# Optimization experiments

Measured on AMD Instinct MI355X. Metric: run time of the kernel, lower is better.

## Reference

```python
import jax, jax.numpy as jnp
import numpy as np

B, S, D = 64, 1024, 128
EPS = 1e-5

def hardswish(x):
    return x * jnp.clip(x + 3.0, 0.0, 6.0) / 6.0

def setup_inputs() -> dict:
    key = jax.random.key(0)
    k1, k2, k3 = jax.random.split(key, 3)
    x = jax.random.normal(k1, (B, S, D), dtype=jnp.float32)
    ln_w = jnp.ones((S, D), dtype=jnp.float32)
    ln_b = jnp.zeros((S, D), dtype=jnp.float32)
    # U1[i]/U2[i] rows packed into lower-triangular (S,S); init ~ N(0,1)*0.01
    W1 = jax.random.normal(k2, (S, S), dtype=jnp.float32) * 0.01
    W2 = jax.random.normal(k3, (S, S), dtype=jnp.float32) * 0.01
    return {"x": x, "ln_w": ln_w, "ln_b": ln_b, "W1": W1, "W2": W2}

def reference(x, ln_w, ln_b, W1, W2):
    # LayerNorm over the last two dims (seq_len, feature_dim) jointly
    mu = jnp.mean(x, axis=(-2, -1), keepdims=True)
    var = jnp.mean(jnp.square(x - mu), axis=(-2, -1), keepdims=True)
    h = (x - mu) * jax.lax.rsqrt(var + EPS) * ln_w + ln_b
    # causal (lower-triangular) time mixing: u[:, t] = sum_{s<=t} W1[t, s] * h[:, s]
    mask = jnp.tril(jnp.ones((S, S), dtype=x.dtype))
    u = hardswish(jnp.einsum('ts,bsd->btd', W1 * mask, h))
    v = jnp.einsum('ts,bsd->btd', W2 * mask, u)
    return x + v
```

## Files before the change

### kernel.cpp

```cpp
#include <hip/hip_runtime.h>
#include <hip/hip_bf16.h>

#define NB 64
#define S_ 1024
#define D_ 128

typedef __attribute__((ext_vector_type(8))) short bf16x8;
typedef __attribute__((ext_vector_type(4))) float f32x4;


__device__ __forceinline__ unsigned short f2bf(float f) {
  __hip_bfloat16 h = __float2bfloat16(f);
  return __builtin_bit_cast(unsigned short, h);
}

__device__ __forceinline__ void async_copy16(const void* g, void* l) {
  __builtin_amdgcn_global_load_lds(
      (const __attribute__((address_space(1))) unsigned int*)g,
      (__attribute__((address_space(3))) unsigned int*)l, 16, 0, 0);
}

__global__ __launch_bounds__(256) void init_stats(unsigned* __restrict__ c) {
#pragma unroll
  for (int i = 0; i < 8; ++i) c[threadIdx.x + i * 256] = 0u;
}

__global__ __launch_bounds__(256) void prep_norm_kernel(
    const float* __restrict__ x, const float* __restrict__ ln_w,
    const float* __restrict__ ln_b, const float* __restrict__ W1,
    const float* __restrict__ W2, float* __restrict__ stats,
    unsigned short* __restrict__ W1f, unsigned short* __restrict__ W2f,
    unsigned short* __restrict__ hTf) {
  __shared__ __align__(16) unsigned short lds[64 * 132 + 32];
  float2* w4 = (float2*)(lds + 64 * 132);
  float* mr = (float*)(lds + 64 * 132 + 16);

  const int blk = blockIdx.x;
  const int b = blk >> 4;
  const int s0 = (blk & 15) * 64;
  const int t = threadIdx.x;
  const int wave = t >> 6, lane = t & 63;
  const int quad = lane >> 4, l16 = lane & 15;

  float* sb = stats + (size_t)b * 32;
  unsigned* cntp = (unsigned*)sb + 2;

  const float4* xb = (const float4*)(x + ((size_t)b * S_ + s0) * D_);
  {
    float s = 0.f, q = 0.f;
#pragma unroll
    for (int i = 0; i < 8; ++i) {
      float4 v = xb[i * 256 + t];
      s += v.x + v.y + v.z + v.w;
      q += v.x * v.x + v.y * v.y + v.z * v.z + v.w * v.w;
    }
#pragma unroll
    for (int o = 32; o > 0; o >>= 1) {
      s += __shfl_down(s, o, 64);
      q += __shfl_down(q, o, 64);
    }
    if (lane == 0) w4[wave] = make_float2(s, q);
  }
  __syncthreads();
  if (t == 0) {
    float ss = 0.f, qq = 0.f;
#pragma unroll
    for (int i = 0; i < 4; ++i) { ss += w4[i].x; qq += w4[i].y; }
    float o1 = __hip_atomic_fetch_add(sb + 0, ss, __ATOMIC_RELAXED,
                                      __HIP_MEMORY_SCOPE_AGENT);
    float o2 = __hip_atomic_fetch_add(sb + 1, qq, __ATOMIC_RELAXED,
                                      __HIP_MEMORY_SCOPE_AGENT);
    asm volatile("" ::"v"(o1), "v"(o2));
    __hip_atomic_fetch_add(cntp, 1u, __ATOMIC_RELAXED,
                           __HIP_MEMORY_SCOPE_AGENT);
  }

  {
    const int u = blk * 4 + wave;
    const int f = u & 2047;
    const int p = f >> 5, c = f & 31;
    const int r = p * 16 + l16;
    const int k0 = c * 32 + quad * 8;
    const float* wsrc = ((u >> 11) ? W2 : W1) + (size_t)r * 1024 + k0;
    float4 a0 = ((const float4*)wsrc)[0];
    float4 a1 = ((const float4*)wsrc)[1];
    float av[8] = {a0.x, a0.y, a0.z, a0.w, a1.x, a1.y, a1.z, a1.w};
    bf16x8 o;
#pragma unroll
    for (int jj = 0; jj < 8; ++jj)
      o[jj] = (short)f2bf((k0 + jj <= r) ? av[jj] : 0.f);
    unsigned short* dstp = ((u >> 11) ? W2f : W1f) +
                           ((size_t)p * 32 + c) * 512 + lane * 8;
    *(bf16x8*)dstp = o;
  }

  if (t == 0) {
    int guard = 0;
    while (__hip_atomic_load(cntp, __ATOMIC_RELAXED,
                             __HIP_MEMORY_SCOPE_AGENT) < 16u) {
      __builtin_amdgcn_s_sleep(4);
      if (++guard > 400000) break;
    }
    float s1 = __hip_atomic_load(sb + 0, __ATOMIC_RELAXED,
                                 __HIP_MEMORY_SCOPE_AGENT);
    float s2 = __hip_atomic_load(sb + 1, __ATOMIC_RELAXED,
                                 __HIP_MEMORY_SCOPE_AGENT);
    const float inv = 1.0f / (S_ * D_);
    const float mu = s1 * inv;
    mr[0] = mu;
    mr[1] = rsqrtf(s2 * inv - mu * mu + 1e-5f);
  }
  __syncthreads();
  const float mu = mr[0];
  const float rs = mr[1];

  const float4* wb = (const float4*)(ln_w + (size_t)s0 * D_);
  const float4* bv4 = (const float4*)(ln_b + (size_t)s0 * D_);
#pragma unroll
  for (int r = 0; r < 8; ++r) {
    const int f = r * 256 + t;
    const int srow = f >> 5;
    const int c4 = f & 31;
    float4 xv = xb[f];
    float4 wv = wb[f];
    float4 bvv = bv4[f];
    ushort4 o;
    o.x = f2bf((xv.x - mu) * rs * wv.x + bvv.x);
    o.y = f2bf((xv.y - mu) * rs * wv.y + bvv.y);
    o.z = f2bf((xv.z - mu) * rs * wv.z + bvv.z);
    o.w = f2bf((xv.w - mu) * rs * wv.w + bvv.w);
    *(ushort4*)(lds + srow * 132 + c4 * 4) = o;
  }
  __syncthreads();
  unsigned short* outp = hTf + (size_t)b * (D_ * S_);
  const int cg0 = (blk & 15) * 2;
#pragma unroll
  for (int ff = 0; ff < 4; ++ff) {
    const int f = wave * 4 + ff;
    const int p = f >> 1, cl = f & 1;
    const int d = p * 16 + l16;
    const int sbase = cl * 32 + quad * 8;
    bf16x8 v;
#pragma unroll
    for (int jj = 0; jj < 8; ++jj)
      v[jj] = (short)lds[(sbase + jj) * 132 + d];
    *(bf16x8*)(outp + ((size_t)p * 32 + cg0 + cl) * 512 + lane * 8) = v;
  }
}

template <bool HSWISH>
__global__ __launch_bounds__(256, 4) void gemm_causal(
    const unsigned short* __restrict__ Af, const unsigned short* __restrict__ Bf,
    unsigned short* __restrict__ Uf, const float* __restrict__ Xres,
    float* __restrict__ Out) {
  __shared__ __align__(16) unsigned short ldsA[16384];

  const int t = threadIdx.x;
  const int wave = t >> 6, lane = t & 63;
  const int quad = lane >> 4, l16 = lane & 15;

  const int bi = blockIdx.x;
  const int xcd = bi & 7;
  const int slot = bi >> 3;
  const int b = xcd * 8 + (slot & 7);
  const int j = slot >> 3;
  const int mt = (j < 8) ? j : (j ^ 3);
  const int row0 = mt * 64;

  const int cend = 2 * (mt + 1);
  const int npan = (cend + 7) >> 3;

  const unsigned short* Ab = Af + (size_t)mt * 4 * 32 * 512;
  const unsigned short* Bb = Bf + (size_t)b * (D_ * S_);

  f32x4 acc[4][2] = {};
  bf16x8 Bp[4][2];
#pragma unroll
  for (int g = 0; g < 4; ++g) {
    const int gg = (g < cend) ? g : 0;
#pragma unroll
    for (int jj = 0; jj < 2; ++jj)
      Bp[g][jj] = *(const bf16x8*)(Bb + ((size_t)(wave * 2 + jj) * 32 + gg) * 512 + lane * 8);
  }

  for (int p = 0; p < npan; ++p) {
    if (p) __syncthreads();
    const int rem = cend - p * 8;
#pragma unroll
    for (int jc = 0; jc < 8; ++jc) {
      const int flat16 = jc * 256 + t;
      const int iw = flat16 >> 9;
      const int cc = (flat16 >> 6) & 7;
      const int li = flat16 & 63;
      if (cc < rem)
        async_copy16(Ab + ((size_t)iw * 32 + p * 8 + cc) * 512 + li * 8,
                     ldsA + flat16 * 8);
    }
    __syncthreads();
#pragma unroll
    for (int c = 0; c < 8; ++c) {
      const int g = p * 8 + c;
      if (g < cend) {
        bf16x8 af[4];
#pragma unroll
        for (int i = 0; i < 4; ++i)
          af[i] = *(const bf16x8*)(ldsA + i * 4096 + c * 512 + lane * 8);
        __builtin_amdgcn_s_setprio(1);
#pragma unroll
        for (int i = 0; i < 4; ++i)
#pragma unroll
          for (int jj = 0; jj < 2; ++jj)
            acc[i][jj] = __builtin_amdgcn_mfma_f32_16x16x32_bf16(
                af[i], Bp[c & 3][jj], acc[i][jj], 0, 0, 0);
        __builtin_amdgcn_s_setprio(0);
        const int gn = (g + 4 < cend) ? (g + 4) : 0;
#pragma unroll
        for (int jj = 0; jj < 2; ++jj)
          Bp[c & 3][jj] = *(const bf16x8*)(
              Bb + ((size_t)(wave * 2 + jj) * 32 + gn) * 512 + lane * 8);
      }
    }
  }

  if (HSWISH) {
    __syncthreads();
    unsigned short* ldsT = ldsA;
#pragma unroll
    for (int i = 0; i < 4; ++i)
#pragma unroll
      for (int jj = 0; jj < 2; ++jj) {
        ushort4 pk;
        float v0 = acc[i][jj][0], v1 = acc[i][jj][1], v2 = acc[i][jj][2], v3 = acc[i][jj][3];
        pk.x = f2bf(v0 * fminf(fmaxf(v0 + 3.f, 0.f), 6.f) * (1.f / 6.f));
        pk.y = f2bf(v1 * fminf(fmaxf(v1 + 3.f, 0.f), 6.f) * (1.f / 6.f));
        pk.z = f2bf(v2 * fminf(fmaxf(v2 + 3.f, 0.f), 6.f) * (1.f / 6.f));
        pk.w = f2bf(v3 * fminf(fmaxf(v3 + 3.f, 0.f), 6.f) * (1.f / 6.f));
        const int n = wave * 32 + jj * 16 + l16;
        const int m0 = i * 16 + quad * 4;
        *(ushort4*)(ldsT + n * 72 + m0) = pk;
      }
    __syncthreads();
    unsigned short* gU = Uf + (size_t)b * (D_ * S_);
#pragma unroll
    for (int ff = 0; ff < 4; ++ff) {
      const int f = wave * 4 + ff;
      const int p2 = f >> 1, cl = f & 1;
      const int d = p2 * 16 + l16;
      const int tb = cl * 32 + quad * 8;
      bf16x8 v = *(const bf16x8*)(ldsT + d * 72 + tb);
      *(bf16x8*)(gU + ((size_t)p2 * 32 + mt * 2 + cl) * 512 + lane * 8) = v;
    }
  } else {
    float* gO = Out + (size_t)b * S_ * D_;
    const float* gX = Xres + (size_t)b * S_ * D_;
#pragma unroll
    for (int i = 0; i < 4; ++i) {
      const int mrow0 = row0 + i * 16 + quad * 4;
#pragma unroll
      for (int jj = 0; jj < 2; ++jj) {
        const int col = wave * 32 + jj * 16 + l16;
#pragma unroll
        for (int r = 0; r < 4; ++r) {
          const int addr = (mrow0 + r) * D_ + col;
          gO[addr] = gX[addr] + acc[i][jj][r];
        }
      }
    }
  }
}

extern "C" void kernel_launch(void* const* d_in, const int* in_sizes, int n_in,
                              void* d_out, int out_size, void* d_ws, size_t ws_size,
                              hipStream_t stream) {
  const float* x = (const float*)d_in[0];
  const float* ln_w = (const float*)d_in[1];
  const float* ln_b = (const float*)d_in[2];
  const float* W1 = (const float*)d_in[3];
  const float* W2 = (const float*)d_in[4];
  float* out = (float*)d_out;

  char* ws = (char*)d_ws;
  float* stats = (float*)ws;
  unsigned short* W1f = (unsigned short*)(ws + 16384);
  unsigned short* W2f = W1f + (size_t)S_ * S_;
  unsigned short* hTf = W2f + (size_t)S_ * S_;
  unsigned short* uTf = hTf + (size_t)NB * D_ * S_;

  init_stats<<<1, 256, 0, stream>>>((unsigned*)stats);
  prep_norm_kernel<<<1024, 256, 0, stream>>>(x, ln_w, ln_b, W1, W2, stats,
                                             W1f, W2f, hTf);
  gemm_causal<true><<<1024, 256, 0, stream>>>(W1f, hTf, uTf, nullptr, nullptr);
  gemm_causal<false><<<1024, 256, 0, stream>>>(W2f, uTf, nullptr, x, out);
}
```

Baseline: 133.4 us.

## Fuse layernorm and both causal GEMMs into one persistent kernel with flag sync

Folds stats init into a separate weight-packing kernel and merges layernorm, the first causal GEMM and the second causal GEMM into a single 1024-block kernel. Blocks coordinate through per-batch bitmasks in global memory: each row tile publishes a bit after writing h or u, and waits only on bits for tiles at or before its own causal row. This removes kernel launch gaps and lets tiles start as soon as their causal dependencies are ready, not after a full grid barrier. It depends on all 1024 blocks being co-resident to avoid deadlock, and relies on sc1 stores plus relaxed atomics for cross-block visibility.

```diff
diff --git a/kernel.cpp b/kernel.cpp
--- a/kernel.cpp
+++ b/kernel.cpp
@@ -7,6 +7,7 @@
 
 typedef __attribute__((ext_vector_type(8))) short bf16x8;
 typedef __attribute__((ext_vector_type(4))) float f32x4;
+typedef __attribute__((ext_vector_type(4))) unsigned int u32x4;
 
 
 __device__ __forceinline__ unsigned short f2bf(float f) {
@@ -20,63 +21,47 @@
       (__attribute__((address_space(3))) unsigned int*)l, 16, 0, 0);
 }
 
-__global__ __launch_bounds__(256) void init_stats(unsigned* __restrict__ c) {
-#pragma unroll
-  for (int i = 0; i < 8; ++i) c[threadIdx.x + i * 256] = 0u;
-}
-
-__global__ __launch_bounds__(256) void prep_norm_kernel(
-    const float* __restrict__ x, const float* __restrict__ ln_w,
-    const float* __restrict__ ln_b, const float* __restrict__ W1,
-    const float* __restrict__ W2, float* __restrict__ stats,
+__device__ __forceinline__ void store16_dev(void* p, bf16x8 v) {
+  u32x4 d = __builtin_bit_cast(u32x4, v);
+  asm volatile("global_store_dwordx4 %0, %1, off sc1" ::"v"(p), "v"(d)
+               : "memory");
+}
+
+__device__ __forceinline__ void spin_mask(unsigned* p, unsigned need) {
+  if (threadIdx.x == 0) {
+    int guard = 0;
+    while ((__hip_atomic_load(p, __ATOMIC_RELAXED, __HIP_MEMORY_SCOPE_AGENT) &
+            need) != need) {
+      __builtin_amdgcn_s_sleep(4);
+      if (++guard > 400000) break;
+    }
+  }
+  __syncthreads();
+  asm volatile("" ::: "memory");
+}
+
+__device__ __forceinline__ void publish_bit(unsigned* p, unsigned bit) {
+  asm volatile("s_waitcnt vmcnt(0)" ::: "memory");
+  __syncthreads();
+  if (threadIdx.x == 0)
+    __hip_atomic_fetch_or(p, bit, __ATOMIC_RELAXED, __HIP_MEMORY_SCOPE_AGENT);
+}
+
+__global__ __launch_bounds__(256) void wpack_kernel(
+    const float* __restrict__ W1, const float* __restrict__ W2,
     unsigned short* __restrict__ W1f, unsigned short* __restrict__ W2f,
-    unsigned short* __restrict__ hTf) {
-  __shared__ __align__(16) unsigned short lds[64 * 132 + 32];
-  float2* w4 = (float2*)(lds + 64 * 132);
-  float* mr = (float*)(lds + 64 * 132 + 16);
-
+    unsigned* __restrict__ stats) {
   const int blk = blockIdx.x;
-  const int b = blk >> 4;
-  const int s0 = (blk & 15) * 64;
   const int t = threadIdx.x;
   const int wave = t >> 6, lane = t & 63;
   const int quad = lane >> 4, l16 = lane & 15;
-
-  float* sb = stats + (size_t)b * 32;
-  unsigned* cntp = (unsigned*)sb + 2;
-
-  const float4* xb = (const float4*)(x + ((size_t)b * S_ + s0) * D_);
-  {
-    float s = 0.f, q = 0.f;
-#pragma unroll
-    for (int i = 0; i < 8; ++i) {
-      float4 v = xb[i * 256 + t];
-      s += v.x + v.y + v.z + v.w;
-      q += v.x * v.x + v.y * v.y + v.z * v.z + v.w * v.w;
-    }
-#pragma unroll
-    for (int o = 32; o > 0; o >>= 1) {
-      s += __shfl_down(s, o, 64);
-      q += __shfl_down(q, o, 64);
-    }
-    if (lane == 0) w4[wave] = make_float2(s, q);
-  }
-  __syncthreads();
-  if (t == 0) {
-    float ss = 0.f, qq = 0.f;
-#pragma unroll
-    for (int i = 0; i < 4; ++i) { ss += w4[i].x; qq += w4[i].y; }
-    float o1 = __hip_atomic_fetch_add(sb + 0, ss, __ATOMIC_RELAXED,
-                                      __HIP_MEMORY_SCOPE_AGENT);
-    float o2 = __hip_atomic_fetch_add(sb + 1, qq, __ATOMIC_RELAXED,
-                                      __HIP_MEMORY_SCOPE_AGENT);
-    asm volatile("" ::"v"(o1), "v"(o2));
-    __hip_atomic_fetch_add(cntp, 1u, __ATOMIC_RELAXED,
-                           __HIP_MEMORY_SCOPE_AGENT);
-  }
-
-  {
-    const int u = blk * 4 + wave;
+  if (blk == 0) {
+#pragma unroll
+    for (int i = 0; i < 8; ++i) stats[t + i * 256] = 0u;
+  }
+#pragma unroll
+  for (int rep = 0; rep < 2; ++rep) {
+    const int u = blk * 8 + wave * 2 + rep;
     const int f = u & 2047;
     const int p = f >> 5, c = f & 31;
     const int r = p * 16 + l16;
@@ -93,78 +78,17 @@
                            ((size_t)p * 32 + c) * 512 + lane * 8;
     *(bf16x8*)dstp = o;
   }
-
-  if (t == 0) {
-    int guard = 0;
-    while (__hip_atomic_load(cntp, __ATOMIC_RELAXED,
-                             __HIP_MEMORY_SCOPE_AGENT) < 16u) {
-      __builtin_amdgcn_s_sleep(4);
-      if (++guard > 400000) break;
-    }
-    float s1 = __hip_atomic_load(sb + 0, __ATOMIC_RELAXED,
-                                 __HIP_MEMORY_SCOPE_AGENT);
-    float s2 = __hip_atomic_load(sb + 1, __ATOMIC_RELAXED,
-                                 __HIP_MEMORY_SCOPE_AGENT);
-    const float inv = 1.0f / (S_ * D_);
-    const float mu = s1 * inv;
-    mr[0] = mu;
-    mr[1] = rsqrtf(s2 * inv - mu * mu + 1e-5f);
-  }
-  __syncthreads();
-  const float mu = mr[0];
-  const float rs = mr[1];
-
-  const float4* wb = (const float4*)(ln_w + (size_t)s0 * D_);
-  const float4* bv4 = (const float4*)(ln_b + (size_t)s0 * D_);
-#pragma unroll
-  for (int r = 0; r < 8; ++r) {
-    const int f = r * 256 + t;
-    const int srow = f >> 5;
-    const int c4 = f & 31;
-    float4 xv = xb[f];
-    float4 wv = wb[f];
-    float4 bvv = bv4[f];
-    ushort4 o;
-    o.x = f2bf((xv.x - mu) * rs * wv.x + bvv.x);
-    o.y = f2bf((xv.y - mu) * rs * wv.y + bvv.y);
-    o.z = f2bf((xv.z - mu) * rs * wv.z + bvv.z);
-    o.w = f2bf((xv.w - mu) * rs * wv.w + bvv.w);
-    *(ushort4*)(lds + srow * 132 + c4 * 4) = o;
-  }
-  __syncthreads();
-  unsigned short* outp = hTf + (size_t)b * (D_ * S_);
-  const int cg0 = (blk & 15) * 2;
-#pragma unroll
-  for (int ff = 0; ff < 4; ++ff) {
-    const int f = wave * 4 + ff;
-    const int p = f >> 1, cl = f & 1;
-    const int d = p * 16 + l16;
-    const int sbase = cl * 32 + quad * 8;
-    bf16x8 v;
-#pragma unroll
-    for (int jj = 0; jj < 8; ++jj)
-      v[jj] = (short)lds[(sbase + jj) * 132 + d];
-    *(bf16x8*)(outp + ((size_t)p * 32 + cg0 + cl) * 512 + lane * 8) = v;
-  }
 }
 
 template <bool HSWISH>
-__global__ __launch_bounds__(256, 4) void gemm_causal(
+__device__ __forceinline__ void gemm_phase(
+    unsigned short* ldsA, const int b, const int mt,
     const unsigned short* __restrict__ Af, const unsigned short* __restrict__ Bf,
     unsigned short* __restrict__ Uf, const float* __restrict__ Xres,
     float* __restrict__ Out) {
-  __shared__ __align__(16) unsigned short ldsA[16384];
-
   const int t = threadIdx.x;
   const int wave = t >> 6, lane = t & 63;
   const int quad = lane >> 4, l16 = lane & 15;
-
-  const int bi = blockIdx.x;
-  const int xcd = bi & 7;
-  const int slot = bi >> 3;
-  const int b = xcd * 8 + (slot & 7);
-  const int j = slot >> 3;
-  const int mt = (j < 8) ? j : (j ^ 3);
   const int row0 = mt * 64;
 
   const int cend = 2 * (mt + 1);
@@ -248,7 +172,7 @@
       const int d = p2 * 16 + l16;
       const int tb = cl * 32 + quad * 8;
       bf16x8 v = *(const bf16x8*)(ldsT + d * 72 + tb);
-      *(bf16x8*)(gU + ((size_t)p2 * 32 + mt * 2 + cl) * 512 + lane * 8) = v;
+      store16_dev(gU + ((size_t)p2 * 32 + mt * 2 + cl) * 512 + lane * 8, v);
     }
   } else {
     float* gO = Out + (size_t)b * S_ * D_;
@@ -267,6 +191,125 @@
       }
     }
   }
+}
+
+__global__ __launch_bounds__(256, 4) void mega_kernel(
+    const float* __restrict__ x, const float* __restrict__ ln_w,
+    const float* __restrict__ ln_b, const unsigned short* __restrict__ W1f,
+    const unsigned short* __restrict__ W2f, float* __restrict__ stats,
+    unsigned short* __restrict__ hTf, unsigned short* __restrict__ uTf,
+    float* __restrict__ out) {
+  __shared__ __align__(16) unsigned short smem[16384];
+
+  const int bi = blockIdx.x;
+  const int xcd = bi & 7;
+  const int slot = bi >> 3;
+  const int b = xcd * 8 + (slot & 7);
+  const int j = slot >> 3;
+  const int mt = (j < 8) ? j : (j ^ 3);
+
+  const int t = threadIdx.x;
+  const int wave = t >> 6, lane = t & 63;
+  const int quad = lane >> 4, l16 = lane & 15;
+
+  float* sb = stats + (size_t)b * 32;
+  unsigned* cntp = (unsigned*)sb + 2;
+  unsigned* hmp = (unsigned*)sb + 4;
+  unsigned* ump = (unsigned*)sb + 6;
+
+  float2* w4 = (float2*)(smem + 8448);
+  float* mr = (float*)(smem + 8464);
+
+  const float4* xb = (const float4*)(x + ((size_t)b * S_ + mt * 64) * D_);
+  {
+    float s = 0.f, q = 0.f;
+#pragma unroll
+    for (int i = 0; i < 8; ++i) {
+      float4 v = xb[i * 256 + t];
+      s += v.x + v.y + v.z + v.w;
+      q += v.x * v.x + v.y * v.y + v.z * v.z + v.w * v.w;
+    }
+#pragma unroll
+    for (int o = 32; o > 0; o >>= 1) {
+      s += __shfl_down(s, o, 64);
+      q += __shfl_down(q, o, 64);
+    }
+    if (lane == 0) w4[wave] = make_float2(s, q);
+  }
+  __syncthreads();
+  if (t == 0) {
+    float ss = 0.f, qq = 0.f;
+#pragma unroll
+    for (int i = 0; i < 4; ++i) { ss += w4[i].x; qq += w4[i].y; }
+    float o1 = __hip_atomic_fetch_add(sb + 0, ss, __ATOMIC_RELAXED,
+                                      __HIP_MEMORY_SCOPE_AGENT);
+    float o2 = __hip_atomic_fetch_add(sb + 1, qq, __ATOMIC_RELAXED,
+                                      __HIP_MEMORY_SCOPE_AGENT);
+    asm volatile("" ::"v"(o1), "v"(o2));
+    __hip_atomic_fetch_add(cntp, 1u, __ATOMIC_RELAXED,
+                           __HIP_MEMORY_SCOPE_AGENT);
+    int guard = 0;
+    while (__hip_atomic_load(cntp, __ATOMIC_RELAXED,
+                             __HIP_MEMORY_SCOPE_AGENT) < 16u) {
+      __builtin_amdgcn_s_sleep(4);
+      if (++guard > 400000) break;
+    }
+    float s1 = __hip_atomic_load(sb + 0, __ATOMIC_RELAXED,
+                                 __HIP_MEMORY_SCOPE_AGENT);
+    float s2 = __hip_atomic_load(sb + 1, __ATOMIC_RELAXED,
+                                 __HIP_MEMORY_SCOPE_AGENT);
+    const float inv = 1.0f / (S_ * D_);
+    const float mu = s1 * inv;
+    mr[0] = mu;
+    mr[1] = rsqrtf(s2 * inv - mu * mu + 1e-5f);
+  }
+  __syncthreads();
+  const float mu = mr[0];
+  const float rs = mr[1];
+
+  {
+    unsigned short* lds = smem;
+    const float4* wb = (const float4*)(ln_w + (size_t)(mt * 64) * D_);
+    const float4* bv4 = (const float4*)(ln_b + (size_t)(mt * 64) * D_);
+#pragma unroll
+    for (int r = 0; r < 8; ++r) {
+      const int f = r * 256 + t;
+      const int srow = f >> 5;
+      const int c4 = f & 31;
+      float4 xv = xb[f];
+      float4 wv = wb[f];
+      float4 bvv = bv4[f];
+      ushort4 o;
+      o.x = f2bf((xv.x - mu) * rs * wv.x + bvv.x);
+      o.y = f2bf((xv.y - mu) * rs * wv.y + bvv.y);
+      o.z = f2bf((xv.z - mu) * rs * wv.z + bvv.z);
+      o.w = f2bf((xv.w - mu) * rs * wv.w + bvv.w);
+      *(ushort4*)(lds + srow * 132 + c4 * 4) = o;
+    }
+    __syncthreads();
+    unsigned short* outp = hTf + (size_t)b * (D_ * S_);
+    const int cg0 = mt * 2;
+#pragma unroll
+    for (int ff = 0; ff < 4; ++ff) {
+      const int f = wave * 4 + ff;
+      const int p = f >> 1, cl = f & 1;
+      const int d = p * 16 + l16;
+      const int sbase = cl * 32 + quad * 8;
+      bf16x8 v;
+#pragma unroll
+      for (int jj = 0; jj < 8; ++jj)
+        v[jj] = (short)lds[(sbase + jj) * 132 + d];
+      store16_dev(outp + ((size_t)p * 32 + cg0 + cl) * 512 + lane * 8, v);
+    }
+  }
+  publish_bit(hmp, 1u << mt);
+
+  spin_mask(hmp, (2u << mt) - 1);
+  gemm_phase<true>(smem, b, mt, W1f, hTf, uTf, nullptr, nullptr);
+  publish_bit(ump, 1u << mt);
+
+  spin_mask(ump, (2u << mt) - 1);
+  gemm_phase<false>(smem, b, mt, W2f, uTf, nullptr, x, out);
 }
 
 extern "C" void kernel_launch(void* const* d_in, const int* in_sizes, int n_in,
@@ -286,9 +329,7 @@
   unsigned short* hTf = W2f + (size_t)S_ * S_;
   unsigned short* uTf = hTf + (size_t)NB * D_ * S_;
 
-  init_stats<<<1, 256, 0, stream>>>((unsigned*)stats);
-  prep_norm_kernel<<<1024, 256, 0, stream>>>(x, ln_w, ln_b, W1, W2, stats,
-                                             W1f, W2f, hTf);
-  gemm_causal<true><<<1024, 256, 0, stream>>>(W1f, hTf, uTf, nullptr, nullptr);
-  gemm_causal<false><<<1024, 256, 0, stream>>>(W2f, uTf, nullptr, x, out);
-}
+  wpack_kernel<<<512, 256, 0, stream>>>(W1, W2, W1f, W2f, (unsigned*)stats);
+  mega_kernel<<<1024, 256, 0, stream>>>(x, ln_w, ln_b, W1f, W2f, stats,
+                                        hTf, uTf, out);
+}
```

Measured after the change: 132.0 us. Within noise of the previous version (-1.0%).
